# Kernel tuning notes

Hardware: AMD Instinct MI355X
Metric: run time of the kernel (lower is better)

The kernel has to match this reference:

```python
import jax, jax.numpy as jnp
import numpy as np
from jax.scipy.special import erf

B, S, D, H, F = 2, 2048, 1024, 16, 4096
EPS = 1e-5


def setup_inputs() -> dict:
    key = jax.random.key(0)
    ks = jax.random.split(key, 7)
    s = 0.02  # init scale so attention logits stay in a sane range
    return {
        "x": jax.random.normal(ks[0], (B, S, D), jnp.float32),
        "wq": jax.random.normal(ks[1], (D, D), jnp.float32) * s,
        "wk": jax.random.normal(ks[2], (D, D), jnp.float32) * s,
        "wv": jax.random.normal(ks[3], (D, D), jnp.float32) * s,
        "wo": jax.random.normal(ks[4], (D, D), jnp.float32) * s,
        "w1": jax.random.normal(ks[5], (F, D), jnp.float32) * s,
        "w2": jax.random.normal(ks[6], (D, F), jnp.float32) * s,
        "g1": jnp.ones((D,), jnp.float32),
        "g2": jnp.ones((D,), jnp.float32),
    }


def _rmsnorm(x, g):
    return x / jnp.sqrt(jnp.mean(x * x, axis=-1, keepdims=True) + EPS) * g


def _gelu_exact(x):
    # 0.5 * x * (1 + erf(x / sqrt(2)))
    return 0.5 * x * (1.0 + erf(x * (1.0 / np.sqrt(2.0).astype(np.float32))))


def reference(x, wq, wk, wv, wo, w1, w2, g1, g2):
    b, s, d = x.shape
    dk = d // H
    # --- attention sublayer (pre-RMSNorm) ---
    h = _rmsnorm(x, g1)
    # Linear(bias=False): y = h @ W.T; split heads -> [b, H, s, dk]
    q = (h @ wq.T).reshape(b, s, H, dk).transpose(0, 2, 1, 3)
    k = (h @ wk.T).reshape(b, s, H, dk).transpose(0, 2, 1, 3)
    v = (h @ wv.T).reshape(b, s, H, dk).transpose(0, 2, 1, 3)
    scores = jnp.einsum('bhqd,bhkd->bhqk', q, k) / jnp.sqrt(jnp.float32(dk))
    causal = jnp.triu(jnp.ones((s, s), bool), 1)  # True above diagonal -> masked
    scores = jnp.where(causal, -jnp.inf, scores)
    attn = jax.nn.softmax(scores, axis=-1)
    o = jnp.einsum('bhqk,bhkd->bhqd', attn, v)
    o = o.transpose(0, 2, 1, 3).reshape(b, s, d) @ wo.T
    x = x + o
    # --- FFN sublayer (pre-RMSNorm, exact-erf GELU) ---
    h2 = _rmsnorm(x, g2)
    f = _gelu_exact(h2 @ w1.T) @ w2.T
    return x + f
```

## Files before the change

kernel.cpp:

```cpp
#include <hip/hip_runtime.h>
#include <hip/hip_bf16.h>
#include <math.h>

#define B_   2
#define S_   2048
#define D_   1024
#define H_   16
#define DK_  64
#define F_   4096
#define NTOK (B_ * S_)

typedef __bf16 bf16x8 __attribute__((ext_vector_type(8)));
typedef float  f32x4  __attribute__((ext_vector_type(4)));

__device__ __forceinline__ unsigned short bf16r(float f) {
  unsigned u = __builtin_bit_cast(unsigned, f);
  u += 0x7fffu + ((u >> 16) & 1u);
  return (unsigned short)(u >> 16);
}

__device__ __forceinline__ void gload_lds16(const void* g, void* l) {
  __builtin_amdgcn_global_load_lds(
      (__attribute__((address_space(1))) void*)g,
      (__attribute__((address_space(3))) void*)l, 16, 0, 0);
}

__device__ __forceinline__ unsigned lds_off(void* p) {
  return (unsigned)(size_t)(__attribute__((address_space(3))) void*)p;
}
__device__ __forceinline__ bf16x8 ds_read16(unsigned a) {
  bf16x8 r;
  asm volatile("ds_read_b128 %0, %1" : "=v"(r) : "v"(a));
  return r;
}
__device__ __forceinline__ void ds_write32(unsigned a, unsigned v) {
  asm volatile("ds_write_b32 %0, %1" : : "v"(a), "v"(v));
}
__device__ __forceinline__ float fexp2(float x) {
  float r;
  asm volatile("v_exp_f32 %0, %1\n\ts_nop 0" : "=v"(r) : "v"(x));
  return r;
}
__device__ __forceinline__ unsigned cvt_pk_bf16(float lo, float hi) {
  unsigned r;
  asm volatile("v_cvt_pk_bf16_f32 %0, %1, %2" : "=v"(r) : "v"(lo), "v"(hi));
  return r;
}

__device__ __forceinline__ float gelu_fast(float x) {
  float y = 0.7978845608f * x * (1.0f + 0.044715f * x * x);
  float e = fexp2(2.885390082f * y);
  float t = 1.0f - 2.0f / (e + 1.0f);
  return 0.5f * x * (1.0f + t);
}

#define QSCL 0.18033688f

struct CvtArgs {
  const float* src[6];
  unsigned short* dst[6];
  int start[7];
};
__global__ __launch_bounds__(256) void cvt_all_kernel(CvtArgs a) {
  int i = blockIdx.x * blockDim.x + threadIdx.x;
  if (i >= a.start[6]) return;
  int k = 0;
#pragma unroll
  for (int j = 1; j < 6; ++j)
    if (i >= a.start[j]) k = j;
  int off = i - a.start[k];
  float4 v = reinterpret_cast<const float4*>(a.src[k])[off];
  ushort4 o;
  o.x = bf16r(v.x); o.y = bf16r(v.y); o.z = bf16r(v.z); o.w = bf16r(v.w);
  reinterpret_cast<ushort4*>(a.dst[k])[off] = o;
}

__global__ __launch_bounds__(256) void rmsnorm_kernel(
    const float* __restrict__ x, const float* __restrict__ g,
    unsigned short* __restrict__ out) {
  int row = blockIdx.x;
  int t = threadIdx.x, lane = t & 63, w = t >> 6;
  float4 v = reinterpret_cast<const float4*>(x + (size_t)row * D_)[t];
  float ss = v.x * v.x + v.y * v.y + v.z * v.z + v.w * v.w;
#pragma unroll
  for (int d = 1; d < 64; d <<= 1) ss += __shfl_xor(ss, d);
  __shared__ float red[4];
  if (lane == 0) red[w] = ss;
  __syncthreads();
  float tot = red[0] + red[1] + red[2] + red[3];
  float rstd = rsqrtf(tot * (1.0f / D_) + 1e-5f);
  float4 gv = reinterpret_cast<const float4*>(g)[t];
  ushort4 o;
  o.x = bf16r(v.x * rstd * gv.x);
  o.y = bf16r(v.y * rstd * gv.y);
  o.z = bf16r(v.z * rstd * gv.z);
  o.w = bf16r(v.w * rstd * gv.w);
  reinterpret_cast<ushort4*>(out + (size_t)row * D_)[t] = o;
}

template <int EPI>
__device__ __forceinline__ void gemm256_body(
    const unsigned short* __restrict__ A, const unsigned short* __restrict__ Bw,
    int M, int N, int K,
    unsigned short* __restrict__ outB, unsigned short* __restrict__ outB2,
    unsigned short* __restrict__ outB3) {
  constexpr int BUFU = 12288;
  __shared__ __attribute__((aligned(16))) unsigned short lds[3 * BUFU];
  const int t = threadIdx.x, lane = t & 63, w = t >> 6;
  const int wm = w >> 1, wn = w & 1;
  const int lg = lane >> 4, ln = lane & 15;

  const int gx = gridDim.x;
  int bid = blockIdx.y * gx + blockIdx.x;
  int xcd = bid & 7, c = bid >> 3;
  int RX = gx >> 2, RY = gridDim.y >> 1;
  int bx = (xcd & 3) * RX + (c % RX);
  int by = (xcd >> 2) * RY + (c / RX);
  const int m0 = by * 256, n0 = bx * 128;

  const int nt = K >> 5;

  auto stage = [&](int tile) {
    int buf = tile % 3;
    const int k0 = tile << 5;
    unsigned short* la = &lds[buf * BUFU];
    unsigned short* lb = la + 8192;
#pragma unroll
    for (int i = 0; i < 2; ++i) {
      int g = i * 512 + t;
      int Ln = g >> 3, p = g & 7, u = p ^ (Ln & 7);
      int row = 2 * Ln + (u >> 2), cg = u & 3;
      gload_lds16(A + (size_t)(m0 + row) * K + k0 + cg * 8, &la[g * 8]);
    }
    {
      int Ln = t >> 3, p = t & 7, u = p ^ (Ln & 7);
      int row = 2 * Ln + (u >> 2), cg = u & 3;
      gload_lds16(Bw + (size_t)(n0 + row) * K + k0 + cg * 8, &lb[t * 8]);
    }
  };

  stage(0);
  stage(1);

  const unsigned base0 = lds_off(lds);
  unsigned offA[4], offB[4];
#pragma unroll
  for (int m = 0; m < 4; ++m) {
    int r = wm * 64 + m * 16 + ln;
    int Ln = r >> 1, p = ((r & 1) * 4 + lg) ^ (Ln & 7);
    offA[m] = (unsigned)((Ln * 64 + p * 8) * 2);
  }
#pragma unroll
  for (int n = 0; n < 4; ++n) {
    int r = wn * 64 + n * 16 + ln;
    int Ln = r >> 1, p = ((r & 1) * 4 + lg) ^ (Ln & 7);
    offB[n] = (unsigned)(16384 + (Ln * 64 + p * 8) * 2);
  }

  f32x4 acc[4][4] = {};

  for (int tile = 0; tile < nt; ++tile) {
    if (tile + 1 < nt) { asm volatile("s_waitcnt vmcnt(3)"); }
    else               { asm volatile("s_waitcnt vmcnt(0)"); }
    __builtin_amdgcn_sched_barrier(0);
    __builtin_amdgcn_s_barrier();
    const unsigned bb = base0 + (unsigned)((tile % 3) * (BUFU * 2));
    bf16x8 af[4], bf0, bf1;
#pragma unroll
    for (int m = 0; m < 4; ++m) af[m] = ds_read16(bb + offA[m]);
    bf0 = ds_read16(bb + offB[0]);
    bf1 = ds_read16(bb + offB[1]);
    if (tile + 2 < nt) stage(tile + 2);
    asm volatile("s_waitcnt lgkmcnt(0)");
    __builtin_amdgcn_sched_barrier(0);
    __builtin_amdgcn_s_setprio(1);
#pragma unroll
    for (int m = 0; m < 4; ++m) {
      acc[m][0] = __builtin_amdgcn_mfma_f32_16x16x32_bf16(af[m], bf0, acc[m][0], 0, 0, 0);
      acc[m][1] = __builtin_amdgcn_mfma_f32_16x16x32_bf16(af[m], bf1, acc[m][1], 0, 0, 0);
    }
    __builtin_amdgcn_s_setprio(0);
    bf0 = ds_read16(bb + offB[2]);
    bf1 = ds_read16(bb + offB[3]);
    asm volatile("s_waitcnt lgkmcnt(0)");
    __builtin_amdgcn_sched_barrier(0);
    __builtin_amdgcn_s_setprio(1);
#pragma unroll
    for (int m = 0; m < 4; ++m) {
      acc[m][2] = __builtin_amdgcn_mfma_f32_16x16x32_bf16(af[m], bf0, acc[m][2], 0, 0, 0);
      acc[m][3] = __builtin_amdgcn_mfma_f32_16x16x32_bf16(af[m], bf1, acc[m][3], 0, 0, 0);
    }
    __builtin_amdgcn_s_setprio(0);
  }

  const int rbase = m0 + wm * 64 + lg * 4;
  const int cbase = n0 + wn * 64 + ln;
#pragma unroll
  for (int m = 0; m < 4; ++m) {
#pragma unroll
    for (int n = 0; n < 4; ++n) {
      int col = cbase + n * 16;
#pragma unroll
      for (int j = 0; j < 4; ++j) {
        int row = rbase + m * 16 + j;
        float v = acc[m][n][j];
        if (EPI == 1) {
          outB[(size_t)row * N + col] = bf16r(gelu_fast(v));
        } else {
          if (col < D_) {
            outB[(size_t)row * D_ + col] = bf16r(v * QSCL);
          } else if (col < 2 * D_) {
            outB2[(size_t)row * D_ + (col - D_)] = bf16r(v);
          } else {
            int bb2 = row >> 11, s = row & (S_ - 1);
            outB3[((size_t)(bb2 * D_) + (col - 2 * D_)) * S_ + s] = bf16r(v);
          }
        }
      }
    }
  }
}

__global__ __launch_bounds__(512, 4) void qkv_gemm(
    const unsigned short* __restrict__ A, const unsigned short* __restrict__ Bw,
    int M, int N, int K, unsigned short* o1, unsigned short* o2, unsigned short* o3) {
  gemm256_body<4>(A, Bw, M, N, K, o1, o2, o3);
}
__global__ __launch_bounds__(512, 4) void ffn1_gemm(
    const unsigned short* __restrict__ A, const unsigned short* __restrict__ Bw,
    int M, int N, int K, unsigned short* o1) {
  gemm256_body<1>(A, Bw, M, N, K, o1, nullptr, nullptr);
}

__device__ __forceinline__ void gemm128_body(
    const unsigned short* __restrict__ A, const unsigned short* __restrict__ Bw,
    int M, int N, int K,
    const float* __restrict__ resid, float* __restrict__ outF) {
  constexpr int BUFU = 256 * 32;
  __shared__ __attribute__((aligned(16))) unsigned short lds[4 * BUFU];
  const int t = threadIdx.x, lane = t & 63, w = t >> 6;
  const int wm = w >> 2, wn = w & 3;
  const int lg = lane >> 4, ln = lane & 15;

  const int gx = gridDim.x;
  int bid = blockIdx.y * gx + blockIdx.x;
  int RX = gx >> 2, RY = gridDim.y >> 1;
  int xcd = bid & 7, c = bid >> 3;
  int bx = (xcd & 3) * RX + (c % RX);
  int by = (xcd >> 2) * RY + (c / RX);
  const int m0 = by * 128, n0 = bx * 128;

  const int nt = K >> 5;

  auto stage = [&](int tile) {
    const int buf = tile & 3;
    const int k0 = tile << 5;
    unsigned short* la = &lds[buf * BUFU];
    unsigned short* lb = la + 4096;
    int Ln = t >> 3, p = t & 7, u = p ^ (Ln & 7);
    int row = 2 * Ln + (u >> 2), cg = u & 3;
    gload_lds16(A + (size_t)(m0 + row) * K + k0 + cg * 8, &la[t * 8]);
    gload_lds16(Bw + (size_t)(n0 + row) * K + k0 + cg * 8, &lb[t * 8]);
  };

  stage(0);
  if (nt > 1) stage(1);
  if (nt > 2) stage(2);

  const unsigned base0 = lds_off(lds);
  unsigned offA[4], offB[2];
#pragma unroll
  for (int m = 0; m < 4; ++m) {
    int r = wm * 64 + m * 16 + ln;
    int Ln = r >> 1, p = ((r & 1) * 4 + lg) ^ (Ln & 7);
    offA[m] = (unsigned)((Ln * 64 + p * 8) * 2);
  }
#pragma unroll
  for (int n = 0; n < 2; ++n) {
    int r = wn * 32 + n * 16 + ln;
    int Ln = r >> 1, p = ((r & 1) * 4 + lg) ^ (Ln & 7);
    offB[n] = (unsigned)(8192 + (Ln * 64 + p * 8) * 2);
  }

  f32x4 acc[4][2] = {};

  for (int tile = 0; tile < nt; ++tile) {
    const int rem = nt - 1 - tile;
    if (rem >= 2)      { asm volatile("s_waitcnt vmcnt(4)"); }
    else if (rem == 1) { asm volatile("s_waitcnt vmcnt(2)"); }
    else               { asm volatile("s_waitcnt vmcnt(0)"); }
    __builtin_amdgcn_sched_barrier(0);
    __builtin_amdgcn_s_barrier();
    const unsigned bb = base0 + (unsigned)((tile & 3) * (BUFU * 2));
    bf16x8 af[4], bf[2];
#pragma unroll
    for (int m = 0; m < 4; ++m) af[m] = ds_read16(bb + offA[m]);
#pragma unroll
    for (int n = 0; n < 2; ++n) bf[n] = ds_read16(bb + offB[n]);
    if (tile + 3 < nt) stage(tile + 3);
    asm volatile("s_waitcnt lgkmcnt(0)");
    __builtin_amdgcn_sched_barrier(0);
    __builtin_amdgcn_s_setprio(1);
#pragma unroll
    for (int m = 0; m < 4; ++m)
#pragma unroll
      for (int n = 0; n < 2; ++n)
        acc[m][n] = __builtin_amdgcn_mfma_f32_16x16x32_bf16(af[m], bf[n], acc[m][n], 0, 0, 0);
    __builtin_amdgcn_s_setprio(0);
  }

  const int rbase = m0 + wm * 64 + lg * 4;
  const int cbase = n0 + wn * 32 + ln;
#pragma unroll
  for (int m = 0; m < 4; ++m) {
#pragma unroll
    for (int n = 0; n < 2; ++n) {
      int col = cbase + n * 16;
#pragma unroll
      for (int j = 0; j < 4; ++j) {
        int row = rbase + m * 16 + j;
        outF[(size_t)row * N + col] = acc[m][n][j] + resid[(size_t)row * N + col];
      }
    }
  }
}

__global__ __launch_bounds__(512, 4) void wo_gemm(
    const unsigned short* __restrict__ A, const unsigned short* __restrict__ Bw,
    int M, int N, int K, const float* __restrict__ resid, float* __restrict__ outF) {
  gemm128_body(A, Bw, M, N, K, resid, outF);
}
__global__ __launch_bounds__(512, 4) void ffn2_gemm(
    const unsigned short* __restrict__ A, const unsigned short* __restrict__ Bw,
    int M, int N, int K, const float* __restrict__ resid, float* __restrict__ outF) {
  gemm128_body(A, Bw, M, N, K, resid, outF);
}

__global__ __launch_bounds__(256, 2) void attn_kernel(
    const unsigned short* __restrict__ qg, const unsigned short* __restrict__ kg,
    const unsigned short* __restrict__ vt, unsigned short* __restrict__ og) {
  __shared__ __attribute__((aligned(16))) unsigned short Kl[2][8192];
  __shared__ __attribute__((aligned(16))) unsigned short Vl[2][8192];
  __shared__ __attribute__((aligned(16))) unsigned short Pl[4][2048];
  const int t = threadIdx.x, lane = t & 63, w = t >> 6;
  const int lg = lane >> 4, ln = lane & 15;

  int bid = blockIdx.x;
  int nl = (bid & 7) * 64 + (bid >> 3);
  int bh = nl >> 4, pi = nl & 15;
  int b = bh >> 4, h = bh & 15;

  const unsigned kbase = lds_off(&Kl[0][0]);
  const unsigned vbase = lds_off(&Vl[0][0]);
  const unsigned pbase = lds_off(&Pl[w][0]);

  auto runq = [&](int qtile, bool first) {
    const int q0 = qtile * 64;
    const int qw = q0 + w * 16;
    const int nt = (q0 >> 7) + 1;

    bf16x8 aq[2];
    {
      const unsigned short* qp =
          qg + (size_t)(b * S_ + qw + ln) * D_ + h * DK_ + lg * 8;
      aq[0] = *reinterpret_cast<const bf16x8*>(qp);
      aq[1] = *reinterpret_cast<const bf16x8*>(qp + 32);
    }
    asm volatile("" : : "v"(aq[0]), "v"(aq[1]));

    float mr = -1e30f, lr = 0.f;
    f32x4 oacc[4] = {};

    auto stage = [&](int kt) {
      const int buf = kt & 1;
      const int kv0 = kt * 128;
#pragma unroll
      for (int i = 0; i < 4; ++i) {
        int g = i * 256 + t;
        int row = g >> 3, cg = g & 7, sg = cg ^ (row & 7);
        gload_lds16(kg + (size_t)(b * S_ + kv0 + row) * D_ + h * DK_ + sg * 8,
                    &Kl[buf][g * 8]);
      }
#pragma unroll
      for (int i = 0; i < 4; ++i) {
        int g = i * 256 + t;
        int row = g >> 4, cg = g & 15, sg = cg ^ (row & 15);
        gload_lds16(vt + (size_t)(b * D_ + h * DK_ + row) * S_ + kv0 + sg * 8,
                    &Vl[buf][g * 8]);
      }
    };

    if (!first) __builtin_amdgcn_s_barrier();
    stage(0);

    auto ctile = [&](int kt, bool dm) {
      const unsigned kb = kbase + (unsigned)((kt & 1) * 16384);
      const unsigned vb = vbase + (unsigned)((kt & 1) * 16384);
      f32x4 sc[8] = {};
      bf16x8 kf[8];
#pragma unroll
      for (int n = 0; n < 8; ++n) {
        int r = n * 16 + ln;
        int cg0 = lg ^ (r & 7);
        kf[n] = ds_read16(kb + (unsigned)((r * 128 + cg0 * 16)));
      }
      if (!dm) stage(kt + 1);
      asm volatile("s_waitcnt lgkmcnt(0)");
      __builtin_amdgcn_sched_barrier(0);
#pragma unroll
      for (int n = 0; n < 8; ++n)
        sc[n] = __builtin_amdgcn_mfma_f32_16x16x32_bf16(kf[n], aq[0], sc[n], 0, 0, 0);
#pragma unroll
      for (int n = 0; n < 8; ++n) {
        int r = n * 16 + ln;
        int cg1 = (4 + lg) ^ (r & 7);
        kf[n] = ds_read16(kb + (unsigned)((r * 128 + cg1 * 16)));
      }
      asm volatile("s_waitcnt lgkmcnt(0)");
      __builtin_amdgcn_sched_barrier(0);
#pragma unroll
      for (int n = 0; n < 8; ++n)
        sc[n] = __builtin_amdgcn_mfma_f32_16x16x32_bf16(kf[n], aq[1], sc[n], 0, 0, 0);
      if (dm) {
        const int kv0 = kt * 128;
        const int qi = qw + ln;
#pragma unroll
        for (int n = 0; n < 8; ++n)
#pragma unroll
          for (int j = 0; j < 4; ++j)
            if ((kv0 + n * 16 + lg * 4 + j) > qi) sc[n][j] = -1e30f;
      }
      float mx = -1e30f;
#pragma unroll
      for (int n = 0; n < 8; ++n) {
        float a = fmaxf(fmaxf(sc[n][0], sc[n][1]), fmaxf(sc[n][2], sc[n][3]));
        mx = fmaxf(mx, a);
      }
      mx = fmaxf(mx, __shfl_xor(mx, 16));
      mx = fmaxf(mx, __shfl_xor(mx, 32));
      float mn = fmaxf(mr, mx);
      float ps = 0.f;
#pragma unroll
      for (int n = 0; n < 8; ++n)
#pragma unroll
        for (int j = 0; j < 4; ++j) {
          float p = fexp2(sc[n][j] - mn);
          sc[n][j] = p;
          ps += p;
        }
      if (__all(mx <= mr)) {
        lr += ps;
      } else {
        float sf = fexp2(mr - mn);
        mr = mn;
        lr = lr * sf + ps;
#pragma unroll
        for (int j = 0; j < 4; ++j) {
          float sfj = __shfl(sf, lg * 4 + j);
#pragma unroll
          for (int f = 0; f < 4; ++f) oacc[f][j] *= sfj;
        }
      }
#pragma unroll
      for (int n = 0; n < 8; ++n) {
        int kvc = n * 16 + lg * 4;
        int gsw = ((kvc >> 3) ^ ln) & 15;
        unsigned pa_addr = pbase + (unsigned)(ln * 256 + gsw * 16 + (kvc & 7) * 2);
        ds_write32(pa_addr, cvt_pk_bf16(sc[n][0], sc[n][1]));
        ds_write32(pa_addr + 4, cvt_pk_bf16(sc[n][2], sc[n][3]));
      }
      asm volatile("s_waitcnt lgkmcnt(0)");
      __builtin_amdgcn_sched_barrier(0);
#pragma unroll
      for (int c = 0; c < 4; ++c) {
        unsigned cgp = (unsigned)(((c * 4 + lg) ^ ln) & 15);
        bf16x8 pa = ds_read16(pbase + (unsigned)(ln * 256) + cgp * 16);
        bf16x8 vf[4];
#pragma unroll
        for (int f = 0; f < 4; ++f) {
          int dv = f * 16 + ln;
          int cgv = ((c * 4 + lg) ^ (dv & 15)) & 15;
          vf[f] = ds_read16(vb + (unsigned)(dv * 256 + cgv * 16));
        }
        asm volatile("s_waitcnt lgkmcnt(0)");
        __builtin_amdgcn_sched_barrier(0);
#pragma unroll
        for (int f = 0; f < 4; ++f)
          oacc[f] = __builtin_amdgcn_mfma_f32_16x16x32_bf16(pa, vf[f], oacc[f], 0, 0, 0);
      }
    };

    for (int kt = 0; kt < nt - 1; ++kt) {
      asm volatile("s_waitcnt vmcnt(0)");
      __builtin_amdgcn_sched_barrier(0);
      __builtin_amdgcn_s_barrier();
      ctile(kt, false);
    }
    asm volatile("s_waitcnt vmcnt(0)");
    __builtin_amdgcn_sched_barrier(0);
    __builtin_amdgcn_s_barrier();
    ctile(nt - 1, true);

    lr += __shfl_xor(lr, 16);
    lr += __shfl_xor(lr, 32);
#pragma unroll
    for (int j = 0; j < 4; ++j) {
      float lj = __shfl(lr, lg * 4 + j);
      float inv = 1.0f / lj;
      int row = b * S_ + qw + lg * 4 + j;
#pragma unroll
      for (int f = 0; f < 4; ++f)
        og[(size_t)row * D_ + h * DK_ + f * 16 + ln] = bf16r(oacc[f][j] * inv);
    }
  };

  runq(31 - pi, true);
  runq(pi, false);
}

extern "C" void kernel_launch(void* const* d_in, const int* in_sizes, int n_in,
                              void* d_out, int out_size, void* d_ws, size_t ws_size,
                              hipStream_t stream) {
  const float* x  = (const float*)d_in[0];
  const float* wq = (const float*)d_in[1];
  const float* wk = (const float*)d_in[2];
  const float* wv = (const float*)d_in[3];
  const float* wo = (const float*)d_in[4];
  const float* w1 = (const float*)d_in[5];
  const float* w2 = (const float*)d_in[6];
  const float* g1 = (const float*)d_in[7];
  const float* g2 = (const float*)d_in[8];
  float* out = (float*)d_out;

  char* ws = (char*)d_ws;
  const size_t MB = 1024 * 1024;
  unsigned short* wqkv_b = (unsigned short*)(ws + 0 * MB);
  unsigned short* wo_b   = (unsigned short*)(ws + 6 * MB);
  unsigned short* w1_b   = (unsigned short*)(ws + 8 * MB);
  unsigned short* w2_b   = (unsigned short*)(ws + 16 * MB);
  unsigned short* h_b    = (unsigned short*)(ws + 24 * MB);
  unsigned short* q_b    = (unsigned short*)(ws + 32 * MB);
  unsigned short* k_b    = (unsigned short*)(ws + 40 * MB);
  unsigned short* vt_b   = (unsigned short*)(ws + 48 * MB);
  unsigned short* o_b    = (unsigned short*)(ws + 56 * MB);
  float*          x1     = (float*)(ws + 64 * MB);
  unsigned short* mid    = (unsigned short*)(ws + 80 * MB);

  CvtArgs ca;
  ca.src[0] = wq; ca.dst[0] = wqkv_b;
  ca.src[1] = wk; ca.dst[1] = wqkv_b + (size_t)D_ * D_;
  ca.src[2] = wv; ca.dst[2] = wqkv_b + (size_t)2 * D_ * D_;
  ca.src[3] = wo; ca.dst[3] = wo_b;
  ca.src[4] = w1; ca.dst[4] = w1_b;
  ca.src[5] = w2; ca.dst[5] = w2_b;
  int q4 = D_ * D_ / 4, f4 = F_ * D_ / 4;
  ca.start[0] = 0;
  ca.start[1] = q4;
  ca.start[2] = 2 * q4;
  ca.start[3] = 3 * q4;
  ca.start[4] = 4 * q4;
  ca.start[5] = 4 * q4 + f4;
  ca.start[6] = 4 * q4 + 2 * f4;
  cvt_all_kernel<<<(ca.start[6] + 255) / 256, 256, 0, stream>>>(ca);

  rmsnorm_kernel<<<NTOK, 256, 0, stream>>>(x, g1, h_b);

  qkv_gemm<<<dim3(3 * D_ / 128, NTOK / 256), dim3(512), 0, stream>>>(
      h_b, wqkv_b, NTOK, 3 * D_, D_, q_b, k_b, vt_b);

  attn_kernel<<<dim3(512), dim3(256), 0, stream>>>(q_b, k_b, vt_b, o_b);

  wo_gemm<<<dim3(D_ / 128, NTOK / 128), dim3(512), 0, stream>>>(
      o_b, wo_b, NTOK, D_, D_, x, x1);

  rmsnorm_kernel<<<NTOK, 256, 0, stream>>>(x1, g2, h_b);

  ffn1_gemm<<<dim3(F_ / 128, NTOK / 256), dim3(512), 0, stream>>>(
      h_b, w1_b, NTOK, F_, D_, mid);

  ffn2_gemm<<<dim3(D_ / 128, NTOK / 128), dim3(512), 0, stream>>>(
      mid, w2_b, NTOK, D_, F_, x1, out);
}
```

Baseline: 227.4 us.

## Split-K the FFN2 GEMM with a reduction kernel and retile QKV GEMM to 128x128

```diff
diff --git a/kernel.cpp b/kernel.cpp
--- a/kernel.cpp
+++ b/kernel.cpp
@@ -98,12 +98,25 @@
   reinterpret_cast<ushort4*>(out + (size_t)row * D_)[t] = o;
 }
 
-template <int EPI>
-__device__ __forceinline__ void gemm256_body(
+__global__ __launch_bounds__(256) void skred_kernel(
+    const float* __restrict__ pb, const float* __restrict__ resid,
+    float* __restrict__ out, int n4) {
+  int i = blockIdx.x * blockDim.x + threadIdx.x;
+  if (i >= n4) return;
+  float4 a = reinterpret_cast<const float4*>(pb)[i];
+  float4 b = reinterpret_cast<const float4*>(pb + (size_t)NTOK * D_)[i];
+  float4 r = reinterpret_cast<const float4*>(resid)[i];
+  float4 o;
+  o.x = a.x + b.x + r.x;
+  o.y = a.y + b.y + r.y;
+  o.z = a.z + b.z + r.z;
+  o.w = a.w + b.w + r.w;
+  reinterpret_cast<float4*>(out)[i] = o;
+}
+
+__global__ __launch_bounds__(512, 4) void ffn1_gemm(
     const unsigned short* __restrict__ A, const unsigned short* __restrict__ Bw,
-    int M, int N, int K,
-    unsigned short* __restrict__ outB, unsigned short* __restrict__ outB2,
-    unsigned short* __restrict__ outB3) {
+    int M, int N, int K, unsigned short* __restrict__ outB) {
   constexpr int BUFU = 12288;
   __shared__ __attribute__((aligned(16))) unsigned short lds[3 * BUFU];
   const int t = threadIdx.x, lane = t & 63, w = t >> 6;
@@ -203,38 +216,125 @@
 #pragma unroll
       for (int j = 0; j < 4; ++j) {
         int row = rbase + m * 16 + j;
+        outB[(size_t)row * N + col] = bf16r(gelu_fast(acc[m][n][j]));
+      }
+    }
+  }
+}
+
+__global__ __launch_bounds__(256, 3) void qkv_gemm(
+    const unsigned short* __restrict__ A, const unsigned short* __restrict__ Bw,
+    int M, int N, int K,
+    unsigned short* __restrict__ outB, unsigned short* __restrict__ outB2,
+    unsigned short* __restrict__ outB3) {
+  constexpr int BUFU = 8192;
+  __shared__ __attribute__((aligned(16))) unsigned short lds[3 * BUFU];
+  const int t = threadIdx.x, lane = t & 63, w = t >> 6;
+  const int wm = w >> 1, wn = w & 1;
+  const int lg = lane >> 4, ln = lane & 15;
+
+  const int gx = gridDim.x;
+  int bid = blockIdx.y * gx + blockIdx.x;
+  int xcd = bid & 7, c = bid >> 3;
+  int RX = gx >> 2, RY = gridDim.y >> 1;
+  int bx = (xcd & 3) * RX + (c % RX);
+  int by = (xcd >> 2) * RY + (c / RX);
+  const int m0 = by * 128, n0 = bx * 128;
+
+  const int nt = K >> 5;
+
+  auto stage = [&](int tile) {
+    int buf = tile % 3;
+    const int k0 = tile << 5;
+    unsigned short* la = &lds[buf * BUFU];
+    unsigned short* lb = la + 4096;
+#pragma unroll
+    for (int i = 0; i < 2; ++i) {
+      int g = i * 256 + t;
+      int Ln = g >> 3, p = g & 7, u = p ^ (Ln & 7);
+      int row = 2 * Ln + (u >> 2), cg = u & 3;
+      gload_lds16(A + (size_t)(m0 + row) * K + k0 + cg * 8, &la[g * 8]);
+    }
+#pragma unroll
+    for (int i = 0; i < 2; ++i) {
+      int g = i * 256 + t;
+      int Ln = g >> 3, p = g & 7, u = p ^ (Ln & 7);
+      int row = 2 * Ln + (u >> 2), cg = u & 3;
+      gload_lds16(Bw + (size_t)(n0 + row) * K + k0 + cg * 8, &lb[g * 8]);
+    }
+  };
+
+  stage(0);
+  stage(1);
+
+  const unsigned base0 = lds_off(lds);
+  unsigned offA[4], offB[4];
+#pragma unroll
+  for (int m = 0; m < 4; ++m) {
+    int r = wm * 64 + m * 16 + ln;
+    int Ln = r >> 1, p = ((r & 1) * 4 + lg) ^ (Ln & 7);
+    offA[m] = (unsigned)((Ln * 64 + p * 8) * 2);
+  }
+#pragma unroll
+  for (int n = 0; n < 4; ++n) {
+    int r = wn * 64 + n * 16 + ln;
+    int Ln = r >> 1, p = ((r & 1) * 4 + lg) ^ (Ln & 7);
+    offB[n] = (unsigned)(8192 + (Ln * 64 + p * 8) * 2);
+  }
+
+  f32x4 acc[4][4] = {};
+
+  for (int tile = 0; tile < nt; ++tile) {
+    if (tile + 1 < nt) { asm volatile("s_waitcnt vmcnt(4)"); }
+    else               { asm volatile("s_waitcnt vmcnt(0)"); }
+    __builtin_amdgcn_sched_barrier(0);
+    __builtin_amdgcn_s_barrier();
+    const unsigned bb = base0 + (unsigned)((tile % 3) * (BUFU * 2));
+    bf16x8 af[4], bf[4];
+#pragma unroll
+    for (int m = 0; m < 4; ++m) af[m] = ds_read16(bb + offA[m]);
+#pragma unroll
+    for (int n = 0; n < 4; ++n) bf[n] = ds_read16(bb + offB[n]);
+    if (tile + 2 < nt) stage(tile + 2);
+    asm volatile("s_waitcnt lgkmcnt(0)");
+    __builtin_amdgcn_sched_barrier(0);
+    __builtin_amdgcn_s_setprio(1);
+#pragma unroll
+    for (int m = 0; m < 4; ++m)
+#pragma unroll
+      for (int n = 0; n < 4; ++n)
+        acc[m][n] = __builtin_amdgcn_mfma_f32_16x16x32_bf16(af[m], bf[n], acc[m][n], 0, 0, 0);
+    __builtin_amdgcn_s_setprio(0);
+  }
+
+  const int rbase = m0 + wm * 64 + lg * 4;
+  const int cbase = n0 + wn * 64 + ln;
+#pragma unroll
+  for (int m = 0; m < 4; ++m) {
+#pragma unroll
+    for (int n = 0; n < 4; ++n) {
+      int col = cbase + n * 16;
+#pragma unroll
+      for (int j = 0; j < 4; ++j) {
+        int row = rbase + m * 16 + j;
         float v = acc[m][n][j];
-        if (EPI == 1) {
-          outB[(size_t)row * N + col] = bf16r(gelu_fast(v));
+        if (col < D_) {
+          outB[(size_t)row * D_ + col] = bf16r(v * QSCL);
+        } else if (col < 2 * D_) {
+          outB2[(size_t)row * D_ + (col - D_)] = bf16r(v);
         } else {
-          if (col < D_) {
-            outB[(size_t)row * D_ + col] = bf16r(v * QSCL);
-          } else if (col < 2 * D_) {
-            outB2[(size_t)row * D_ + (col - D_)] = bf16r(v);
-          } else {
-            int bb2 = row >> 11, s = row & (S_ - 1);
-            outB3[((size_t)(bb2 * D_) + (col - 2 * D_)) * S_ + s] = bf16r(v);
-          }
+          int bb2 = row >> 11, s = row & (S_ - 1);
+          outB3[((size_t)(bb2 * D_) + (col - 2 * D_)) * S_ + s] = bf16r(v);
         }
       }
     }
   }
 }
 
-__global__ __launch_bounds__(512, 4) void qkv_gemm(
-    const unsigned short* __restrict__ A, const unsigned short* __restrict__ Bw,
-    int M, int N, int K, unsigned short* o1, unsigned short* o2, unsigned short* o3) {
-  gemm256_body<4>(A, Bw, M, N, K, o1, o2, o3);
-}
-__global__ __launch_bounds__(512, 4) void ffn1_gemm(
-    const unsigned short* __restrict__ A, const unsigned short* __restrict__ Bw,
-    int M, int N, int K, unsigned short* o1) {
-  gemm256_body<1>(A, Bw, M, N, K, o1, nullptr, nullptr);
-}
-
+template <int SPLITK>
 __device__ __forceinline__ void gemm128_body(
     const unsigned short* __restrict__ A, const unsigned short* __restrict__ Bw,
-    int M, int N, int K,
+    int M, int N, int K, int koff, int klen,
     const float* __restrict__ resid, float* __restrict__ outF) {
   constexpr int BUFU = 256 * 32;
   __shared__ __attribute__((aligned(16))) unsigned short lds[4 * BUFU];
@@ -250,11 +350,11 @@
   int by = (xcd >> 2) * RY + (c / RX);
   const int m0 = by * 128, n0 = bx * 128;
 
-  const int nt = K >> 5;
+  const int nt = klen >> 5;
 
   auto stage = [&](int tile) {
     const int buf = tile & 3;
-    const int k0 = tile << 5;
+    const int k0 = koff + (tile << 5);
     unsigned short* la = &lds[buf * BUFU];
     unsigned short* lb = la + 4096;
     int Ln = t >> 3, p = t & 7, u = p ^ (Ln & 7);
@@ -319,7 +419,11 @@
 #pragma unroll
       for (int j = 0; j < 4; ++j) {
         int row = rbase + m * 16 + j;
-        outF[(size_t)row * N + col] = acc[m][n][j] + resid[(size_t)row * N + col];
+        if (SPLITK == 0) {
+          outF[(size_t)row * N + col] = acc[m][n][j] + resid[(size_t)row * N + col];
+        } else {
+          outF[(size_t)row * N + col] = acc[m][n][j];
+        }
       }
     }
   }
@@ -328,12 +432,14 @@
 __global__ __launch_bounds__(512, 4) void wo_gemm(
     const unsigned short* __restrict__ A, const unsigned short* __restrict__ Bw,
     int M, int N, int K, const float* __restrict__ resid, float* __restrict__ outF) {
-  gemm128_body(A, Bw, M, N, K, resid, outF);
-}
-__global__ __launch_bounds__(512, 4) void ffn2_gemm(
+  gemm128_body<0>(A, Bw, M, N, K, 0, K, resid, outF);
+}
+__global__ __launch_bounds__(512, 4) void ffn2_gemm_sk(
     const unsigned short* __restrict__ A, const unsigned short* __restrict__ Bw,
-    int M, int N, int K, const float* __restrict__ resid, float* __restrict__ outF) {
-  gemm128_body(A, Bw, M, N, K, resid, outF);
+    int M, int N, int K, float* __restrict__ pb) {
+  const int kz = blockIdx.z;
+  gemm128_body<1>(A, Bw, M, N, K, kz * (K >> 1), K >> 1, nullptr,
+                  pb + (size_t)kz * M * N);
 }
 
 __global__ __launch_bounds__(256, 2) void attn_kernel(
@@ -545,6 +651,7 @@
   unsigned short* o_b    = (unsigned short*)(ws + 56 * MB);
   float*          x1     = (float*)(ws + 64 * MB);
   unsigned short* mid    = (unsigned short*)(ws + 80 * MB);
+  float*          pb     = (float*)(ws + 24 * MB);
 
   CvtArgs ca;
   ca.src[0] = wq; ca.dst[0] = wqkv_b;
@@ -565,7 +672,7 @@
 
   rmsnorm_kernel<<<NTOK, 256, 0, stream>>>(x, g1, h_b);
 
-  qkv_gemm<<<dim3(3 * D_ / 128, NTOK / 256), dim3(512), 0, stream>>>(
+  qkv_gemm<<<dim3(3 * D_ / 128, NTOK / 128), dim3(256), 0, stream>>>(
       h_b, wqkv_b, NTOK, 3 * D_, D_, q_b, k_b, vt_b);
 
   attn_kernel<<<dim3(512), dim3(256), 0, stream>>>(q_b, k_b, vt_b, o_b);
@@ -578,6 +685,9 @@
   ffn1_gemm<<<dim3(F_ / 128, NTOK / 256), dim3(512), 0, stream>>>(
       h_b, w1_b, NTOK, F_, D_, mid);
 
-  ffn2_gemm<<<dim3(D_ / 128, NTOK / 128), dim3(512), 0, stream>>>(
-      mid, w2_b, NTOK, D_, F_, x1, out);
-}
+  ffn2_gemm_sk<<<dim3(D_ / 128, NTOK / 128, 2), dim3(512), 0, stream>>>(
+      mid, w2_b, NTOK, D_, F_, pb);
+
+  skred_kernel<<<(NTOK * D_ / 4 + 255) / 256, 256, 0, stream>>>(
+      pb, x1, out, NTOK * D_ / 4);
+}
```

New measurement: 230.9 us. About the same (+1.5%).
